# Performance work log

Hardware: AMD Instinct MI355X
Metric: run time of the kernel (lower is better)

## Reference

```python
import jax, jax.numpy as jnp
import numpy as np

N_EMBD = 1024
N_HEAD = 16

def setup_inputs() -> dict:
    key = jax.random.key(0)
    ks = jax.random.split(key, 6)
    C = N_EMBD
    s = 1.0 / np.sqrt(C)
    x = jax.random.normal(ks[0], (4, 2048, C), dtype=jnp.float32)
    Wk = jax.random.normal(ks[1], (C, C), dtype=jnp.float32) * s
    Wq = jax.random.normal(ks[2], (C, C), dtype=jnp.float32) * s
    Wv = jax.random.normal(ks[3], (C, C), dtype=jnp.float32) * s
    Wp = jax.random.normal(ks[4], (C, C), dtype=jnp.float32) * s
    bp = jax.random.normal(ks[5], (C,), dtype=jnp.float32) * 0.01
    return {"x": x, "Wq": Wq, "Wk": Wk, "Wv": Wv, "Wp": Wp, "bp": bp}

def reference(x, Wq, Wk, Wv, Wp, bp):
    B, T, C = x.shape
    H = N_HEAD
    d = C // H
    # projections (bias=False)
    q = (x @ Wq).reshape(B, T, H, d).transpose(0, 2, 1, 3)  # [B,H,T,d]
    k = (x @ Wk).reshape(B, T, H, d).transpose(0, 2, 1, 3)
    v = (x @ Wv).reshape(B, T, H, d).transpose(0, 2, 1, 3)
    att = jnp.einsum('bhqd,bhkd->bhqk', q, k) * (1.0 / np.sqrt(d))
    causal = jnp.tril(jnp.ones((T, T), dtype=bool))
    att = jnp.where(causal[None, None], att, jnp.float32(-jnp.inf))
    att = jax.nn.softmax(att, axis=-1)
    y = jnp.einsum('bhqk,bhkd->bhqd', att, v)  # [B,H,T,d]
    y = y.transpose(0, 2, 1, 3).reshape(B, T, C)
    return y @ Wp + bp
```

## Files before the change

### kernel.cpp

```cpp
#include <hip/hip_runtime.h>
#include <hip/hip_bf16.h>

#define N_EMBD 1024
#define N_HEADS 16
#define HD 64
#define TSEQ 2048
#define BATCH 4
#define M_TOT (BATCH*TSEQ)

typedef short s16x8 __attribute__((ext_vector_type(8)));
typedef float f32x4 __attribute__((ext_vector_type(4)));

__device__ __forceinline__ void glds16(const void* g, void* l) {
  __builtin_amdgcn_global_load_lds((const __attribute__((address_space(1))) void*)g,
                                   (__attribute__((address_space(3))) void*)l, 16, 0, 0);
}

__device__ __forceinline__ float exp_scaled(float s) {
  float r;
  asm("v_exp_f32 %0, %1\n\ts_nop 0" : "=v"(r) : "v"(s * 0.18033688011112042f));
  return r;
}

__device__ __forceinline__ unsigned cvtpk(float lo, float hi) {
  unsigned r;
  asm("v_cvt_pk_bf16_f32 %0, %1, %2" : "=v"(r) : "v"(lo), "v"(hi));
  return r;
}

__global__ __launch_bounds__(256) void xcast_kernel(const float* __restrict__ x,
                                                    __hip_bfloat16* __restrict__ xb) {
  int i = blockIdx.x * 256 + threadIdx.x;
  float4 f = ((const float4*)x)[i];
  __hip_bfloat162 p0, p1;
  p0.x = __float2bfloat16(f.x); p0.y = __float2bfloat16(f.y);
  p1.x = __float2bfloat16(f.z); p1.y = __float2bfloat16(f.w);
  ((__hip_bfloat162*)xb)[2*i]   = p0;
  ((__hip_bfloat162*)xb)[2*i+1] = p1;
}

__global__ void wcast_kernel(const float* __restrict__ Wq, const float* __restrict__ Wk,
                             const float* __restrict__ Wv, const float* __restrict__ Wp,
                             __hip_bfloat16* __restrict__ wqkvt, __hip_bfloat16* __restrict__ wpt) {
  __shared__ float tile[32][33];
  int z = blockIdx.z;
  const float* in = (z==0)?Wq:(z==1)?Wk:(z==2)?Wv:Wp;
  __hip_bfloat16* out = (z<3) ? (wqkvt + (size_t)z*N_EMBD*N_EMBD) : wpt;
  int tx = threadIdx.x, ty = threadIdx.y;
  int x  = blockIdx.x*32 + tx;
  int y0 = blockIdx.y*32;
  #pragma unroll
  for (int j=0;j<4;++j) tile[ty + j*8][tx] = in[(size_t)(y0+ty+j*8)*N_EMBD + x];
  __syncthreads();
  int xo  = y0 + tx;
  int yo0 = blockIdx.x*32;
  #pragma unroll
  for (int j=0;j<4;++j)
    out[(size_t)(yo0+ty+j*8)*N_EMBD + xo] = __float2bfloat16(tile[tx][ty+j*8]);
}

__global__ __launch_bounds__(512, 2) void gemm256_kernel(
    const __hip_bfloat16* __restrict__ A,
    const __hip_bfloat16* __restrict__ Bt,
    __hip_bfloat16* __restrict__ Qb, __hip_bfloat16* __restrict__ Kb,
    __hip_bfloat16* __restrict__ Vt) {
  __shared__ __align__(16) char smem[131072];
  int tid = threadIdx.x;
  int nb = blockIdx.x;
  int m0 = blockIdx.y * 256;
  const __hip_bfloat16* Asrc = A  + (size_t)m0 * N_EMBD;
  const __hip_bfloat16* Bsrc = Bt + (size_t)nb * 256 * N_EMBD;

  int lane = tid & 63, wv = tid >> 6, l16 = lane & 15, quad = lane >> 4;
  int swr = wv >> 2, swc = wv & 3;
  int xg = l16 & 7;
  int offc0 = ((quad    ) ^ xg) * 8;
  int offc1 = ((quad + 4) ^ xg) * 8;
  int r0  = tid >> 3;
  int gsw = ((tid & 7) ^ (r0 & 7)) * 8;
  int gln = (tid & 7) * 8;

  f32x4 acc[8][4];
  #pragma unroll
  for (int mi=0;mi<8;++mi)
    #pragma unroll
    for (int ni=0;ni<4;++ni) acc[mi][ni] = (f32x4){0.f,0.f,0.f,0.f};

#define STG(srcbase, kk, hh_, dst_) do {                                      \
    const __hip_bfloat16* s_ = (srcbase) + (size_t)((hh_)*128 + r0)*N_EMBD + (kk) + gsw; \
    __hip_bfloat16* d_ = (dst_) + (hh_)*8192 + r0*64 + gln;                   \
    glds16(s_, d_);                                                           \
    glds16(s_ + (size_t)64*N_EMBD, d_ + 64*64);                               \
  } while (0)

  {
    __hip_bfloat16* A0b = (__hip_bfloat16*)smem;
    __hip_bfloat16* B0b = (__hip_bfloat16*)(smem + 32768);
    STG(Asrc, 0, 0, A0b);
    STG(Bsrc, 0, 0, B0b);
    STG(Asrc, 0, 1, A0b);
    STG(Bsrc, 0, 1, B0b);
  }

  for (int t = 0; t < 16; ++t) {
    int kn = t*64 + 64;
    char* cb   = smem + (size_t)(t & 1) * 65536;
    char* nbuf = smem + (size_t)((t + 1) & 1) * 65536;
    const __hip_bfloat16* Acur = (const __hip_bfloat16*)cb;
    const __hip_bfloat16* Bcur = (const __hip_bfloat16*)(cb + 32768);
    __hip_bfloat16* An = (__hip_bfloat16*)nbuf;
    __hip_bfloat16* Bn = (__hip_bfloat16*)(nbuf + 32768);

    if (t < 15) {
      STG(Asrc, kn, 0, An);
      STG(Bsrc, kn, 0, Bn);
      STG(Asrc, kn, 1, An);
      STG(Bsrc, kn, 1, Bn);
      asm volatile("s_waitcnt vmcnt(8)" ::: "memory");
    } else {
      asm volatile("s_waitcnt vmcnt(0)" ::: "memory");
    }
    __builtin_amdgcn_s_barrier();
    __builtin_amdgcn_sched_barrier(0);

    s16x8 af[8][2], bq[4][2];
    #pragma unroll
    for (int ni=0; ni<4; ++ni) {
      const __hip_bfloat16* p_ = Bcur + (swc*64 + ni*16 + l16)*64;
      bq[ni][0] = *(const s16x8*)(p_ + offc0);
      bq[ni][1] = *(const s16x8*)(p_ + offc1);
    }
    #pragma unroll
    for (int mi=0; mi<8; ++mi) {
      const __hip_bfloat16* p_ = Acur + (swr*128 + mi*16 + l16)*64;
      af[mi][0] = *(const s16x8*)(p_ + offc0);
      af[mi][1] = *(const s16x8*)(p_ + offc1);
    }
    #pragma unroll
    for (int mi=0; mi<8; ++mi)
      #pragma unroll
      for (int ni=0; ni<4; ++ni) {
        acc[mi][ni] = __builtin_amdgcn_mfma_f32_16x16x32_bf16(af[mi][0], bq[ni][0], acc[mi][ni],0,0,0);
        acc[mi][ni] = __builtin_amdgcn_mfma_f32_16x16x32_bf16(af[mi][1], bq[ni][1], acc[mi][ni],0,0,0);
      }

    asm volatile("s_waitcnt lgkmcnt(0)" ::: "memory");
    __builtin_amdgcn_s_barrier();
    __builtin_amdgcn_sched_barrier(0);
  }
#undef STG

  int which = nb >> 2;
  int bb = m0 >> 11, t0 = m0 & 2047;
  if (which < 2) {
    __hip_bfloat16* outp = (which==0)?Qb:Kb;
    int nloc = (nb & 3) * 256;
    #pragma unroll
    for (int mi=0;mi<8;++mi)
      #pragma unroll
      for (int ni=0;ni<4;++ni) {
        int col = nloc + swc*64 + ni*16 + l16;
        int hh = col >> 6, dd = col & 63;
        int trow = t0 + swr*128 + mi*16 + quad*4;
        __hip_bfloat16* dst = outp + ((size_t)(bb*N_HEADS + hh)*TSEQ + trow)*HD + dd;
        #pragma unroll
        for (int r=0;r<4;++r)
          dst[(size_t)r*HD] = __float2bfloat16(acc[mi][ni][r]);
      }
  } else {
    int hh0 = (nb & 3) * 4;
    __hip_bfloat16 (*Ts)[264] = (__hip_bfloat16(*)[264])smem;
    #pragma unroll
    for (int hd=0; hd<4; ++hd) {
      if (hd) __builtin_amdgcn_s_barrier();
      if (swc == hd) {
        #pragma unroll
        for (int mi=0;mi<8;++mi)
          #pragma unroll
          for (int ni=0;ni<4;++ni) {
            int dd = ni*16 + l16;
            int trow = swr*128 + mi*16 + quad*4;
            #pragma unroll
            for (int r=0;r<4;++r)
              Ts[dd][trow + r] = __float2bfloat16(acc[mi][ni][r]);
          }
      }
      __syncthreads();
      int dd = tid >> 3, tcb = (tid & 7) * 32;
      __hip_bfloat16* dst = Vt + ((size_t)(bb*N_HEADS + hh0 + hd)*HD + dd)*TSEQ + t0;
      #pragma unroll
      for (int pb=0; pb<8; ++pb) {
        int q  = tcb + pb*4;
        int pp = q & 63;
        int key = (q & 192) | (pp & 32) | ((pp & 4) << 2) | ((pp & 24) >> 1);
        *(uint2*)(dst + q) = *(const uint2*)&Ts[dd][key];
      }
    }
  }
}

__global__ __launch_bounds__(256) void gemm_kernel(
    const __hip_bfloat16* __restrict__ A,
    const __hip_bfloat16* __restrict__ Bt,
    __hip_bfloat16* __restrict__ Qb, __hip_bfloat16* __restrict__ Kb,
    __hip_bfloat16* __restrict__ Vt,
    float* __restrict__ out, const float* __restrict__ bias, int mode) {
  __shared__ __align__(16) char smem[32768];
  __hip_bfloat16* Alin = (__hip_bfloat16*)smem;
  __hip_bfloat16* Blin = (__hip_bfloat16*)(smem + 16384);
  int tid = threadIdx.x;
  int m0 = blockIdx.y*128, n0 = blockIdx.x*128;
  int w = tid>>6, lane = tid&63, l16 = lane&15, quad = lane>>4;
  int wr = w>>1, wc = w&1;
  int xg = l16 & 7;
  int off0 = ((quad    ) ^ xg)*8;
  int off1 = ((quad + 4) ^ xg)*8;
  f32x4 acc[4][4];
  #pragma unroll
  for (int mi=0;mi<4;++mi)
    #pragma unroll
    for (int ni=0;ni<4;++ni) acc[mi][ni] = (f32x4){0.f,0.f,0.f,0.f};

  for (int k0=0; k0<N_EMBD; k0+=64) {
    __syncthreads();
    #pragma unroll
    for (int rd=0; rd<4; ++rd) {
      int slot = rd*256 + tid;
      int row  = slot>>3;
      int gc8  = ((tid&7) ^ (row&7))*8;
      glds16(A  + (size_t)(m0+row)*N_EMBD + k0 + gc8, Alin + slot*8);
      glds16(Bt + (size_t)(n0+row)*N_EMBD + k0 + gc8, Blin + slot*8);
    }
    __syncthreads();
    #pragma unroll
    for (int c=0;c<2;++c) {
      int off = c ? off1 : off0;
      s16x8 af[4], bfr[4];
      #pragma unroll
      for (int mi=0;mi<4;++mi)
        af[mi] = *(const s16x8*)(Alin + (wr*64+mi*16+l16)*64 + off);
      #pragma unroll
      for (int ni=0;ni<4;++ni)
        bfr[ni] = *(const s16x8*)(Blin + (wc*64+ni*16+l16)*64 + off);
      #pragma unroll
      for (int mi=0;mi<4;++mi)
        #pragma unroll
        for (int ni=0;ni<4;++ni)
          acc[mi][ni] = __builtin_amdgcn_mfma_f32_16x16x32_bf16(af[mi], bfr[ni], acc[mi][ni],0,0,0);
    }
  }

  if (mode == 0) {
  } else {
    #pragma unroll
    for (int mi=0;mi<4;++mi) {
      #pragma unroll
      for (int ni=0;ni<4;++ni) {
        int col = n0 + wc*64 + ni*16 + l16;
        float bs = bias[col];
        #pragma unroll
        for (int r=0;r<4;++r) {
          int m = m0 + wr*64 + mi*16 + quad*4 + r;
          out[(size_t)m*N_EMBD + col] = acc[mi][ni][r] + bs;
        }
      }
    }
  }
}

__global__ __launch_bounds__(256) void attn_kernel(
    const __hip_bfloat16* __restrict__ Qb, const __hip_bfloat16* __restrict__ Kb,
    const __hip_bfloat16* __restrict__ Vt, __hip_bfloat16* __restrict__ Yb) {
  __shared__ __align__(16) __hip_bfloat16 Ks[2][64][64];
  __shared__ __align__(16) __hip_bfloat16 Vs[2][64][64];
  int tid = threadIdx.x;
  int wgid = blockIdx.x;
  int qb = (int)((0x01237564AB89CDEFull >> ((wgid>>6)*4)) & 15);
  int h  = (wgid>>2) & 15;
  int b  = wgid & 3;
  int q0 = qb*128;
  size_t bhT  = (size_t)(b*N_HEADS + h)*TSEQ;
  size_t bhHD = (size_t)(b*N_HEADS + h)*HD;
  int lane = tid&63, w = tid>>6, l16 = lane&15, quad = lane>>4;
  int wq = w*32;
  int xg = l16 & 7;
  int off0 = ((quad    ) ^ xg)*8;
  int off1 = ((quad + 4) ^ xg)*8;

  int slot0 = tid,        row0 = slot0>>3, gcA = ((tid&7) ^ (row0&7))*8;
  int slot1 = 256 + tid,  row1 = slot1>>3, gcB = ((tid&7) ^ (row1&7))*8;

  s16x8 qf[2][2];
  #pragma unroll
  for (int mi=0;mi<2;++mi) {
    const __hip_bfloat16* qrow = Qb + (bhT + q0 + wq + mi*16 + l16)*HD;
    qf[mi][0] = *(const s16x8*)(qrow + quad*8);
    qf[mi][1] = *(const s16x8*)(qrow + 32 + quad*8);
  }

  f32x4 z4 = {0.f,0.f,0.f,0.f};
  f32x4 oacc[4][2];
  #pragma unroll
  for (int nd=0;nd<4;++nd) { oacc[nd][0]=z4; oacc[nd][1]=z4; }
  float lsum[2] = {0.f, 0.f};

  int ntiles = 2*qb + 2;

  {
    glds16(Kb + (bhT + 0 + row0)*HD + gcA,    &Ks[0][0][0] + slot0*8);
    glds16(Vt + (bhHD + row0)*TSEQ + 0 + gcA, &Vs[0][0][0] + slot0*8);
    glds16(Kb + (bhT + 0 + row1)*HD + gcB,    &Ks[0][0][0] + slot1*8);
    glds16(Vt + (bhHD + row1)*TSEQ + 0 + gcB, &Vs[0][0][0] + slot1*8);
  }

  for (int t=0; t<ntiles; ++t) {
    int cur = t&1;
    int k0 = t*64;
    if (t+1 < ntiles) {
      int kn = k0 + 64;
      glds16(Kb + (bhT + kn + row0)*HD + gcA,     &Ks[cur^1][0][0] + slot0*8);
      glds16(Vt + (bhHD + row0)*TSEQ + kn + gcA,  &Vs[cur^1][0][0] + slot0*8);
      glds16(Kb + (bhT + kn + row1)*HD + gcB,     &Ks[cur^1][0][0] + slot1*8);
      glds16(Vt + (bhHD + row1)*TSEQ + kn + gcB,  &Vs[cur^1][0][0] + slot1*8);
      asm volatile("s_waitcnt vmcnt(4)" ::: "memory");
    } else {
      asm volatile("s_waitcnt vmcnt(0)" ::: "memory");
    }
    __builtin_amdgcn_s_barrier();
    __builtin_amdgcn_sched_barrier(0);

    const __hip_bfloat16* Kc = &Ks[cur][0][0];
    const __hip_bfloat16* Vc = &Vs[cur][0][0];

    f32x4 sacc[4][2];
    #pragma unroll
    for (int ni=0; ni<4; ++ni) {
      s16x8 kb0 = *(const s16x8*)(Kc + (ni*16+l16)*64 + off0);
      s16x8 kb1 = *(const s16x8*)(Kc + (ni*16+l16)*64 + off1);
      #pragma unroll
      for (int mi=0; mi<2; ++mi) {
        f32x4 s = z4;
        s = __builtin_amdgcn_mfma_f32_16x16x32_bf16(kb0, qf[mi][0], s,0,0,0);
        s = __builtin_amdgcn_mfma_f32_16x16x32_bf16(kb1, qf[mi][1], s,0,0,0);
        sacc[ni][mi] = s;
      }
    }

    unsigned pkw[2][4][2];
    if (q0 + wq >= k0 + 63) {
      #pragma unroll
      for (int ni=0; ni<4; ++ni) {
        #pragma unroll
        for (int mi=0; mi<2; ++mi) {
          float e0 = exp_scaled(sacc[ni][mi][0]);
          float e1 = exp_scaled(sacc[ni][mi][1]);
          float e2 = exp_scaled(sacc[ni][mi][2]);
          float e3 = exp_scaled(sacc[ni][mi][3]);
          lsum[mi] += (e0+e1)+(e2+e3);
          pkw[mi][ni][0] = cvtpk(e0, e1);
          pkw[mi][ni][1] = cvtpk(e2, e3);
        }
      }
    } else {
      #pragma unroll
      for (int ni=0; ni<4; ++ni) {
        int kbase = k0 + ni*16 + quad*4;
        #pragma unroll
        for (int mi=0; mi<2; ++mi) {
          int qrow = q0 + wq + mi*16 + l16;
          float e0 = (qrow >= kbase    ) ? exp_scaled(sacc[ni][mi][0]) : 0.f;
          float e1 = (qrow >= kbase + 1) ? exp_scaled(sacc[ni][mi][1]) : 0.f;
          float e2 = (qrow >= kbase + 2) ? exp_scaled(sacc[ni][mi][2]) : 0.f;
          float e3 = (qrow >= kbase + 3) ? exp_scaled(sacc[ni][mi][3]) : 0.f;
          lsum[mi] += (e0+e1)+(e2+e3);
          pkw[mi][ni][0] = cvtpk(e0, e1);
          pkw[mi][ni][1] = cvtpk(e2, e3);
        }
      }
    }

    union U8 { s16x8 v; unsigned u[4]; };
    U8 pf[2][2];
    #pragma unroll
    for (int c=0; c<2; ++c)
      #pragma unroll
      for (int mi=0; mi<2; ++mi) {
        pf[c][mi].u[0] = pkw[mi][2*c  ][0];
        pf[c][mi].u[1] = pkw[mi][2*c  ][1];
        pf[c][mi].u[2] = pkw[mi][2*c+1][0];
        pf[c][mi].u[3] = pkw[mi][2*c+1][1];
      }
    #pragma unroll
    for (int nd=0; nd<4; ++nd) {
      const __hip_bfloat16* vrow = Vc + (nd*16 + l16)*64;
      s16x8 vb0 = *(const s16x8*)(vrow + off0);
      s16x8 vb1 = *(const s16x8*)(vrow + off1);
      oacc[nd][0] = __builtin_amdgcn_mfma_f32_16x16x32_bf16(vb0, pf[0][0].v, oacc[nd][0],0,0,0);
      oacc[nd][1] = __builtin_amdgcn_mfma_f32_16x16x32_bf16(vb0, pf[0][1].v, oacc[nd][1],0,0,0);
      oacc[nd][0] = __builtin_amdgcn_mfma_f32_16x16x32_bf16(vb1, pf[1][0].v, oacc[nd][0],0,0,0);
      oacc[nd][1] = __builtin_amdgcn_mfma_f32_16x16x32_bf16(vb1, pf[1][1].v, oacc[nd][1],0,0,0);
    }

    asm volatile("s_waitcnt lgkmcnt(0)" ::: "memory");
    __builtin_amdgcn_s_barrier();
    __builtin_amdgcn_sched_barrier(0);
  }

  #pragma unroll
  for (int mi=0; mi<2; ++mi) {
    lsum[mi] += __shfl_xor(lsum[mi], 16);
    lsum[mi] += __shfl_xor(lsum[mi], 32);
  }

  #pragma unroll
  for (int mi=0; mi<2; ++mi) {
    float inv = 1.f / lsum[mi];
    int tq = q0 + wq + mi*16 + l16;
    __hip_bfloat16* yr = Yb + ((size_t)(b*TSEQ + tq))*N_EMBD + h*HD + quad*4;
    #pragma unroll
    for (int nd=0; nd<4; ++nd) {
      uint2 o;
      o.x = cvtpk(oacc[nd][mi][0]*inv, oacc[nd][mi][1]*inv);
      o.y = cvtpk(oacc[nd][mi][2]*inv, oacc[nd][mi][3]*inv);
      *(uint2*)(yr + nd*16) = o;
    }
  }
}

extern "C" void kernel_launch(void* const* d_in, const int* in_sizes, int n_in,
                              void* d_out, int out_size, void* d_ws, size_t ws_size,
                              hipStream_t stream) {
  const float* x  = (const float*)d_in[0];
  const float* Wq = (const float*)d_in[1];
  const float* Wk = (const float*)d_in[2];
  const float* Wv = (const float*)d_in[3];
  const float* Wp = (const float*)d_in[4];
  const float* bp = (const float*)d_in[5];

  char* w = (char*)d_ws;
  __hip_bfloat16* xb    = (__hip_bfloat16*)w;  w += (size_t)M_TOT*N_EMBD*2;
  __hip_bfloat16* wqkvt = (__hip_bfloat16*)w;  w += (size_t)3*N_EMBD*N_EMBD*2;
  __hip_bfloat16* wpt   = (__hip_bfloat16*)w;  w += (size_t)N_EMBD*N_EMBD*2;
  __hip_bfloat16* Qb    = (__hip_bfloat16*)w;  w += (size_t)M_TOT*N_EMBD*2;
  __hip_bfloat16* Kb    = (__hip_bfloat16*)w;  w += (size_t)M_TOT*N_EMBD*2;
  __hip_bfloat16* Vt    = (__hip_bfloat16*)w;  w += (size_t)M_TOT*N_EMBD*2;
  __hip_bfloat16* Yb    = (__hip_bfloat16*)w;

  xcast_kernel<<<dim3(M_TOT*N_EMBD/1024), dim3(256), 0, stream>>>(x, xb);
  wcast_kernel<<<dim3(32,32,4), dim3(32,8), 0, stream>>>(Wq,Wk,Wv,Wp,wqkvt,wpt);
  gemm256_kernel<<<dim3(12,32), dim3(512), 0, stream>>>(xb, wqkvt, Qb,Kb,Vt);
  attn_kernel<<<dim3(1024), dim3(256), 0, stream>>>(Qb,Kb,Vt,Yb);
  gemm_kernel<<<dim3(8,64), dim3(256), 0, stream>>>(Yb, wpt, nullptr,nullptr,nullptr,
                                                    (float*)d_out, bp, 1);
}
```

Before: 240.8 us.

## Deepen QKV GEMM prefetch with a five-slot LDS ring of half-tiles

The QKV projection GEMM drops its two-buffer LDS scheme for a five-slot ring of 32KB half-tiles (A and B rows for one 128-row half). Loads are issued about two and a half K-steps ahead, with the vmcnt waits adjusted to match. The goal is to hide more global-to-LDS latency behind the MFMA work. The cost is that LDS use rises to 160KB and the slot indexing becomes more involved. A cosmetic rewrite of the mode check in the projection kernel is also included.

Result: no change. 242.9 us (+0.9%).

```diff
diff --git a/kernel.cpp b/kernel.cpp
--- a/kernel.cpp
+++ b/kernel.cpp
@@ -64,7 +64,7 @@
     const __hip_bfloat16* __restrict__ Bt,
     __hip_bfloat16* __restrict__ Qb, __hip_bfloat16* __restrict__ Kb,
     __hip_bfloat16* __restrict__ Vt) {
-  __shared__ __align__(16) char smem[131072];
+  __shared__ __align__(16) char smem[163840];
   int tid = threadIdx.x;
   int nb = blockIdx.x;
   int m0 = blockIdx.y * 256;
@@ -86,36 +86,31 @@
     #pragma unroll
     for (int ni=0;ni<4;++ni) acc[mi][ni] = (f32x4){0.f,0.f,0.f,0.f};
 
-#define STG(srcbase, kk, hh_, dst_) do {                                      \
-    const __hip_bfloat16* s_ = (srcbase) + (size_t)((hh_)*128 + r0)*N_EMBD + (kk) + gsw; \
-    __hip_bfloat16* d_ = (dst_) + (hh_)*8192 + r0*64 + gln;                   \
-    glds16(s_, d_);                                                           \
-    glds16(s_ + (size_t)64*N_EMBD, d_ + 64*64);                               \
+#define STGC(sl_, tt_, hh_) do {                                              \
+    __hip_bfloat16* db = (__hip_bfloat16*)smem + (size_t)(sl_)*16384;         \
+    const __hip_bfloat16* sA = Asrc + (size_t)((hh_)*128 + r0)*N_EMBD + (tt_)*64 + gsw; \
+    glds16(sA,                     db + r0*64 + gln);                         \
+    glds16(sA + (size_t)64*N_EMBD, db + (64+r0)*64 + gln);                    \
+    const __hip_bfloat16* sB = Bsrc + (size_t)((hh_)*128 + r0)*N_EMBD + (tt_)*64 + gsw; \
+    glds16(sB,                     db + 8192 + r0*64 + gln);                  \
+    glds16(sB + (size_t)64*N_EMBD, db + 8192 + (64+r0)*64 + gln);             \
   } while (0)
 
-  {
-    __hip_bfloat16* A0b = (__hip_bfloat16*)smem;
-    __hip_bfloat16* B0b = (__hip_bfloat16*)(smem + 32768);
-    STG(Asrc, 0, 0, A0b);
-    STG(Bsrc, 0, 0, B0b);
-    STG(Asrc, 0, 1, A0b);
-    STG(Bsrc, 0, 1, B0b);
-  }
-
+  STGC(0, 0, 0);
+  STGC(1, 0, 1);
+  STGC(2, 1, 0);
+
+  int s0 = 0;
   for (int t = 0; t < 16; ++t) {
-    int kn = t*64 + 64;
-    char* cb   = smem + (size_t)(t & 1) * 65536;
-    char* nbuf = smem + (size_t)((t + 1) & 1) * 65536;
-    const __hip_bfloat16* Acur = (const __hip_bfloat16*)cb;
-    const __hip_bfloat16* Bcur = (const __hip_bfloat16*)(cb + 32768);
-    __hip_bfloat16* An = (__hip_bfloat16*)nbuf;
-    __hip_bfloat16* Bn = (__hip_bfloat16*)(nbuf + 32768);
-
-    if (t < 15) {
-      STG(Asrc, kn, 0, An);
-      STG(Bsrc, kn, 0, Bn);
-      STG(Asrc, kn, 1, An);
-      STG(Bsrc, kn, 1, Bn);
+    int s1 = s0 + 1; if (s1 >= 5) s1 -= 5;
+    int sa = s0 + 3; if (sa >= 5) sa -= 5;
+    int sb = s0 + 4; if (sb >= 5) sb -= 5;
+    if (t <= 13) {
+      STGC(sa, t+1, 1);
+      STGC(sb, t+2, 0);
+      asm volatile("s_waitcnt vmcnt(12)" ::: "memory");
+    } else if (t == 14) {
+      STGC(sa, 15, 1);
       asm volatile("s_waitcnt vmcnt(8)" ::: "memory");
     } else {
       asm volatile("s_waitcnt vmcnt(0)" ::: "memory");
@@ -123,16 +118,20 @@
     __builtin_amdgcn_s_barrier();
     __builtin_amdgcn_sched_barrier(0);
 
+    const __hip_bfloat16* Ach = (const __hip_bfloat16*)smem + (size_t)(swr ? s1 : s0)*16384;
+    const __hip_bfloat16* Bch = (const __hip_bfloat16*)smem + (size_t)((swc>>1) ? s1 : s0)*16384 + 8192;
+    int bl = (swc & 1) * 64;
+
     s16x8 af[8][2], bq[4][2];
     #pragma unroll
     for (int ni=0; ni<4; ++ni) {
-      const __hip_bfloat16* p_ = Bcur + (swc*64 + ni*16 + l16)*64;
+      const __hip_bfloat16* p_ = Bch + (bl + ni*16 + l16)*64;
       bq[ni][0] = *(const s16x8*)(p_ + offc0);
       bq[ni][1] = *(const s16x8*)(p_ + offc1);
     }
     #pragma unroll
     for (int mi=0; mi<8; ++mi) {
-      const __hip_bfloat16* p_ = Acur + (swr*128 + mi*16 + l16)*64;
+      const __hip_bfloat16* p_ = Ach + (mi*16 + l16)*64;
       af[mi][0] = *(const s16x8*)(p_ + offc0);
       af[mi][1] = *(const s16x8*)(p_ + offc1);
     }
@@ -147,8 +146,9 @@
     asm volatile("s_waitcnt lgkmcnt(0)" ::: "memory");
     __builtin_amdgcn_s_barrier();
     __builtin_amdgcn_sched_barrier(0);
-  }
-#undef STG
+    s0 += 2; if (s0 >= 5) s0 -= 5;
+  }
+#undef STGC
 
   int which = nb >> 2;
   int bb = m0 >> 11, t0 = m0 & 2047;
@@ -250,8 +250,7 @@
     }
   }
 
-  if (mode == 0) {
-  } else {
+  if (mode == 1) {
     #pragma unroll
     for (int mi=0;mi<4;++mi) {
       #pragma unroll
```
